# Optimization experiments

Measured on AMD Instinct MI355X. Metric: run time of the kernel, lower is better.

The kernel has to match this reference:

```python
import jax, jax.numpy as jnp
import numpy as np
import math

FACTOR = 5


def setup_inputs() -> dict:
    key = jax.random.key(0)
    k1, k2, k3, k4 = jax.random.split(key, 4)
    B, L, H, D = 8, 1024, 8, 64
    S = FACTOR * math.ceil(math.log(L))  # U_part = 35
    return {
        "queries": jax.random.normal(k1, (B, L, H, D), jnp.float32),
        "keys": jax.random.normal(k2, (B, L, H, D), jnp.float32),
        "values": jax.random.normal(k3, (B, L, H, D), jnp.float32),
        "sample_idx": jax.random.randint(k4, (L, S), 0, L, dtype=jnp.int32),
        "attn_mask": 0,  # unused by the original forward
    }


def reference(queries, keys, values, sample_idx, attn_mask):
    B, L_Q, H, D = queries.shape
    L_K = keys.shape[1]
    # [B, L, H, D] -> [B, H, L, D]
    Q = jnp.transpose(queries, (0, 2, 1, 3))
    K = jnp.transpose(keys, (0, 2, 1, 3))
    V = jnpp_transpose(values) if False else jnp.transpose(values, (0, 2, 1, 3))

    u = min(FACTOR * math.ceil(math.log(L_Q)), L_Q)  # n_top

    # --- _prob_QK: sampled scores, sparsity measure, top-u query selection ---
    K_sample = K[:, :, sample_idx, :]  # [B, H, L_Q, S, D]
    QK_sample = jnp.einsum('bhqd,bhqsd->bhqs', Q, K_sample)  # [B, H, L_Q, S]
    M = QK_sample.max(axis=-1) - QK_sample.sum(axis=-1) / L_K  # [B, H, L_Q]
    _, M_top = jax.lax.top_k(M, u)  # [B, H, u]

    Q_reduce = jnp.take_along_axis(Q, M_top[..., None], axis=2)  # [B, H, u, D]
    scale = 1.0 / math.sqrt(D)
    scores_top = jnp.einsum('bhud,bhkd->bhuk', Q_reduce, K) * scale  # [B, H, u, L_K]

    # --- initial context (mask_flag=True): running causal mean of V ---
    denom = jnp.arange(1, L_K + 1, dtype=V.dtype)[:, None]  # [L_K, 1]
    context = jnp.cumsum(V, axis=2) / denom  # [B, H, L_K, D]

    # --- softmax over keys, sparse update of selected query rows ---
    attn = jax.nn.softmax(scores_top, axis=-1)  # [B, H, u, L_K]
    update = jnp.einsum('bhuk,bhkd->bhud', attn, V)  # [B, H, u, D]

    b_idx = jnp.arange(B)[:, None, None]
    h_idx = jnp.arange(H)[None, :, None]
    context = context.at[b_idx, h_idx, M_top].set(update)

    return jnp.transpose(context, (0, 2, 1, 3))  # [B, L_Q, H, D]
```

## Files before the change

kernel.cpp:

```cpp
#include <hip/hip_runtime.h>
#include <math.h>

#define BB 8
#define LL 1024
#define HH 8
#define DD 64
#define SS 35
#define UU 35
#define BH (BB*HH)
#define CH 32
#define CROWS (LL/CH)
#define NCHK 4
#define CHK 256
#define RPAD 48

#define MBLOCKS 16384
#define C1BLOCKS (BH*CH)

typedef __attribute__((ext_vector_type(8))) short short8;
typedef __attribute__((ext_vector_type(4))) float f32x4;

__device__ __forceinline__ size_t qkv_off(int b, int l, int h, int d) {
    return (((size_t)b*LL + l)*HH + h)*DD + d;
}

__device__ __forceinline__ unsigned short f2bf(float x) {
    unsigned int u = __float_as_uint(x);
    u = (u + 0x7fffu + ((u >> 16) & 1u)) >> 16;
    return (unsigned short)u;
}

__device__ __forceinline__ short8 ld_bf8_g(const float* __restrict__ p) {
    float4 x = *reinterpret_cast<const float4*>(p);
    float4 y = *reinterpret_cast<const float4*>(p + 4);
    short8 r;
    r[0] = (short)f2bf(x.x); r[1] = (short)f2bf(x.y);
    r[2] = (short)f2bf(x.z); r[3] = (short)f2bf(x.w);
    r[4] = (short)f2bf(y.x); r[5] = (short)f2bf(y.y);
    r[6] = (short)f2bf(y.z); r[7] = (short)f2bf(y.w);
    return r;
}

__global__ __launch_bounds__(256, 4) void kernel_M_csum1(const float* __restrict__ Q,
                                                         const float* __restrict__ K,
                                                         const float* __restrict__ V,
                                                         const int*   __restrict__ sidx,
                                                         float* __restrict__ M,
                                                         float* __restrict__ csum) {
    int blk = blockIdx.x;
    if (blk < MBLOCKS) {
        int xcd  = blk & 7;
        int slot = blk >> 3;
        int bh   = ((slot >> 8) << 3) | xcd;
        int j    = slot & 255;
        int widx = threadIdx.x >> 6, lane = threadIdx.x & 63;
        int q = j * 4 + widx;
        int b = bh >> 3, h = bh & 7;
        int sub = lane & 15, grp = lane >> 4;

        const f32x4 q4 = *reinterpret_cast<const f32x4*>(Q + qkv_off(b, q, h, sub * 4));
        const int* si = sidx + q * SS;

        int idxv[9];
#pragma unroll
        for (int i = 0; i < 9; i++) {
            int s = i * 4 + grp;
            idxv[i] = si[s < SS ? s : 0];
        }
        asm volatile("" : "+v"(idxv[0]), "+v"(idxv[1]), "+v"(idxv[2]),
                          "+v"(idxv[3]), "+v"(idxv[4]), "+v"(idxv[5]),
                          "+v"(idxv[6]), "+v"(idxv[7]), "+v"(idxv[8]));

        f32x4 kv[9];
#pragma unroll
        for (int i = 0; i < 9; i++)
            kv[i] = *reinterpret_cast<const f32x4*>(K + qkv_off(b, idxv[i], h, sub * 4));
        asm volatile("" : "+v"(kv[0]), "+v"(kv[1]), "+v"(kv[2]),
                          "+v"(kv[3]), "+v"(kv[4]), "+v"(kv[5]),
                          "+v"(kv[6]), "+v"(kv[7]), "+v"(kv[8]));

        float mx = -INFINITY, sm = 0.f;
#pragma unroll
        for (int i = 0; i < 9; i++) {
            float p = q4.x * kv[i].x + q4.y * kv[i].y + q4.z * kv[i].z + q4.w * kv[i].w;
            p += __shfl_xor(p, 1);
            p += __shfl_xor(p, 2);
            p += __shfl_xor(p, 4);
            p += __shfl_xor(p, 8);
            if (i * 4 + grp < SS) { mx = fmaxf(mx, p); sm += p; }
        }
        mx = fmaxf(mx, __shfl_xor(mx, 16)); sm += __shfl_xor(sm, 16);
        mx = fmaxf(mx, __shfl_xor(mx, 32)); sm += __shfl_xor(sm, 32);
        if (lane == 0) M[bh * LL + q] = mx - sm * (1.0f / LL);
    } else {
        int blk2 = blk - MBLOCKS;
        int bh = blk2 >> 5, c = blk2 & (CH - 1);
        int b = bh >> 3, h = bh & 7;
        int d = threadIdx.x & 63, seg = threadIdx.x >> 6;
        int l0 = c * CROWS + seg * (CROWS / 4);
        const float* vp = V + qkv_off(b, l0, h, d);
        float vr[CROWS / 4];
#pragma unroll
        for (int i = 0; i < CROWS / 4; i++) vr[i] = vp[(size_t)i * (HH * DD)];
        float s = 0.f;
#pragma unroll
        for (int i = 0; i < CROWS / 4; i++) s += vr[i];
        __shared__ float red[4][64];
        red[seg][d] = s;
        __syncthreads();
        if (seg == 0)
            csum[(size_t)blk2 * 64 + d] = red[0][d] + red[1][d] + red[2][d] + red[3][d];
    }
}

__global__ __launch_bounds__(64, 4) void kernel_topk_csum2(const float* __restrict__ M,
                                                           int* __restrict__ top,
                                                           const float* __restrict__ V,
                                                           const float* __restrict__ csum,
                                                           float* __restrict__ out) {
    if (blockIdx.x < BH) {
        int bh = blockIdx.x, lane = threadIdx.x;
        float v[16];
#pragma unroll
        for (int i = 0; i < 16; i++) v[i] = M[bh * LL + i * 64 + lane];

        for (int k = 0; k < UU; k++) {
            float bv = -INFINITY; int bi = 0x7fffffff;
#pragma unroll
            for (int i = 0; i < 16; i++) {
                if (v[i] > bv) { bv = v[i]; bi = i * 64 + lane; }
            }
#pragma unroll
            for (int w = 1; w < 64; w <<= 1) {
                float ov = __shfl_xor(bv, w);
                int   oi = __shfl_xor(bi, w);
                if (ov > bv || (ov == bv && oi < bi)) { bv = ov; bi = oi; }
            }
            if (lane == 0) top[bh * UU + k] = bi;
            if ((bi & 63) == lane) {
                int slot = bi >> 6;
#pragma unroll
                for (int i = 0; i < 16; i++) if (i == slot) v[i] = -INFINITY;
            }
        }
    } else {
        int blk = blockIdx.x - BH;
        int bh = blk >> 5, c = blk & (CH - 1);
        int b = bh >> 3, h = bh & 7;
        int d = threadIdx.x;
        int l0 = c * CROWS;
        const float* vp = V + qkv_off(b, l0, h, d);

        float vr[CROWS];
#pragma unroll
        for (int i = 0; i < CROWS; i++) vr[i] = vp[(size_t)i * (HH * DD)];

        float prefix = 0.f;
#pragma unroll
        for (int cc = 0; cc < CH; cc++) {
            float vv = csum[(size_t)(bh * CH + cc) * 64 + d];
            prefix += (cc < c) ? vv : 0.f;
        }
        float* op = out + qkv_off(b, l0, h, d);
        float run = prefix;
#pragma unroll
        for (int i = 0; i < CROWS; i++) {
            run += vr[i];
            op[(size_t)i * (HH * DD)] = run / (float)(l0 + i + 1);
        }
    }
}

__global__ __launch_bounds__(256) void kernel_attn_part(const float* __restrict__ Q,
                                                        const float* __restrict__ K,
                                                        const float* __restrict__ V,
                                                        const int*   __restrict__ top,
                                                        float* __restrict__ m_ws,
                                                        float* __restrict__ se_ws,
                                                        float* __restrict__ pv_ws) {
    __shared__ unsigned short vt[64 * CHK];
    __shared__ unsigned short p_lds[RPAD * CHK];
    __shared__ float red_m[4][RPAD];
    __shared__ float red_se[4][RPAD];
    __shared__ int   qpos_s[RPAD];

    const int blk = blockIdx.x;
    const int bh  = blk >> 2;
    const int ch  = blk & 3;
    const int b   = bh >> 3, h = bh & 7;
    const int l0  = ch * CHK;
    const int tid = threadIdx.x;
    const int w    = tid >> 6;
    const int lane = tid & 63;
    const int c    = lane & 15;
    const int g    = lane >> 4;
    const float scale = 0.125f;

    if (tid < RPAD) qpos_s[tid] = top[bh * UU + (tid < UU ? tid : UU - 1)];

#pragma unroll
    for (int i = 0; i < 8; i++) {
        int task = i * 256 + tid;
        int d   = task & 63;
        int lq8 = task >> 6;
        float vv[8];
#pragma unroll
        for (int j = 0; j < 8; j++)
            vv[j] = V[qkv_off(b, l0 + lq8 * 8 + j, h, d)];
        short8 pk;
#pragma unroll
        for (int j = 0; j < 8; j++) pk[j] = (short)f2bf(vv[j]);
        *reinterpret_cast<short8*>(vt + d * CHK + (((lq8 ^ (d & 31)) << 3))) = pk;
    }
    __syncthreads();

    f32x4 acc[3][4];
#pragma unroll
    for (int mt = 0; mt < 3; mt++)
#pragma unroll
        for (int nt = 0; nt < 4; nt++) acc[mt][nt] = (f32x4){0.f, 0.f, 0.f, 0.f};

#pragma unroll
    for (int ks = 0; ks < 2; ks++) {
        int k0 = ks * 32 + g * 8;
        short8 af[3];
#pragma unroll
        for (int mt = 0; mt < 3; mt++) {
            int row = mt * 16 + c;
            af[mt] = ld_bf8_g(Q + qkv_off(b, qpos_s[row], h, k0));
        }
#pragma unroll
        for (int nt = 0; nt < 4; nt++) {
            int kl = l0 + w * 64 + nt * 16 + c;
            short8 bf = ld_bf8_g(K + qkv_off(b, kl, h, k0));
#pragma unroll
            for (int mt = 0; mt < 3; mt++)
                acc[mt][nt] = __builtin_amdgcn_mfma_f32_16x16x32_bf16(af[mt], bf, acc[mt][nt], 0, 0, 0);
        }
    }

    float tmax[3][4];
#pragma unroll
    for (int mt = 0; mt < 3; mt++)
#pragma unroll
        for (int r = 0; r < 4; r++) {
            float m = fmaxf(fmaxf(acc[mt][0][r], acc[mt][1][r]),
                            fmaxf(acc[mt][2][r], acc[mt][3][r]));
            m = fmaxf(m, __shfl_xor(m, 1));
            m = fmaxf(m, __shfl_xor(m, 2));
            m = fmaxf(m, __shfl_xor(m, 4));
            m = fmaxf(m, __shfl_xor(m, 8));
            tmax[mt][r] = m;
        }
    if (c == 0) {
#pragma unroll
        for (int mt = 0; mt < 3; mt++)
#pragma unroll
            for (int r = 0; r < 4; r++)
                red_m[w][mt * 16 + g * 4 + r] = tmax[mt][r];
    }
    __syncthreads();

    float tse[3][4];
#pragma unroll
    for (int mt = 0; mt < 3; mt++)
#pragma unroll
        for (int r = 0; r < 4; r++) {
            int row = mt * 16 + g * 4 + r;
            float m = fmaxf(fmaxf(red_m[0][row], red_m[1][row]),
                            fmaxf(red_m[2][row], red_m[3][row]));
            float s = 0.f;
#pragma unroll
            for (int nt = 0; nt < 4; nt++) {
                float p = __expf(scale * (acc[mt][nt][r] - m));
                acc[mt][nt][r] = p;
                s += p;
                p_lds[row * CHK + w * 64 + nt * 16 + c] = f2bf(p);
            }
            s += __shfl_xor(s, 1);
            s += __shfl_xor(s, 2);
            s += __shfl_xor(s, 4);
            s += __shfl_xor(s, 8);
            tse[mt][r] = s;
        }
    if (c == 0) {
#pragma unroll
        for (int mt = 0; mt < 3; mt++)
#pragma unroll
            for (int r = 0; r < 4; r++)
                red_se[w][mt * 16 + g * 4 + r] = tse[mt][r];
    }
    __syncthreads();

    if (tid < RPAD) {
        float mm = fmaxf(fmaxf(red_m[0][tid], red_m[1][tid]),
                         fmaxf(red_m[2][tid], red_m[3][tid]));
        float ss = red_se[0][tid] + red_se[1][tid] + red_se[2][tid] + red_se[3][tid];
        m_ws[blk * RPAD + tid]  = mm;
        se_ws[blk * RPAD + tid] = ss;
    }

    f32x4 acc2[3];
#pragma unroll
    for (int mt = 0; mt < 3; mt++) acc2[mt] = (f32x4){0.f, 0.f, 0.f, 0.f};

#pragma unroll
    for (int ks = 0; ks < 8; ks++) {
        int slot = ks * 4 + g;
        int d    = w * 16 + c;
        short8 bf = *reinterpret_cast<const short8*>(
            vt + d * CHK + ((slot ^ (d & 31)) << 3));
#pragma unroll
        for (int mt = 0; mt < 3; mt++) {
            short8 af = *reinterpret_cast<const short8*>(
                p_lds + (mt * 16 + c) * CHK + ks * 32 + g * 8);
            acc2[mt] = __builtin_amdgcn_mfma_f32_16x16x32_bf16(af, bf, acc2[mt], 0, 0, 0);
        }
    }

#pragma unroll
    for (int mt = 0; mt < 3; mt++)
#pragma unroll
        for (int r = 0; r < 4; r++) {
            int row = mt * 16 + g * 4 + r;
            pv_ws[((size_t)blk * RPAD + row) * 64 + w * 16 + c] = acc2[mt][r];
        }
}

__global__ __launch_bounds__(256) void kernel_attn_comb(const int* __restrict__ top,
                                                        const float* __restrict__ m_ws,
                                                        const float* __restrict__ se_ws,
                                                        const float* __restrict__ pv_ws,
                                                        float* __restrict__ out) {
    int bh = blockIdx.x;
    int b = bh >> 3, h = bh & 7;
    const float scale = 0.125f;
    for (int idx = threadIdx.x; idx < UU * 64; idx += 256) {
        int r = idx >> 6, d = idx & 63;
        float mc[NCHK];
        float mm = -INFINITY;
#pragma unroll
        for (int ch = 0; ch < NCHK; ch++) {
            mc[ch] = m_ws[(bh * NCHK + ch) * RPAD + r];
            mm = fmaxf(mm, mc[ch]);
        }
        float num = 0.f, den = 0.f;
#pragma unroll
        for (int ch = 0; ch < NCHK; ch++) {
            float f = __expf(scale * (mc[ch] - mm));
            num += f * pv_ws[((size_t)(bh * NCHK + ch) * RPAD + r) * 64 + d];
            den += f * se_ws[(bh * NCHK + ch) * RPAD + r];
        }
        out[qkv_off(b, top[bh * UU + r], h, d)] = num / den;
    }
}

extern "C" void kernel_launch(void* const* d_in, const int* in_sizes, int n_in,
                              void* d_out, int out_size, void* d_ws, size_t ws_size,
                              hipStream_t stream) {
    const float* Q    = (const float*)d_in[0];
    const float* K    = (const float*)d_in[1];
    const float* V    = (const float*)d_in[2];
    const int*   sidx = (const int*)d_in[3];
    float* out = (float*)d_out;

    char* ws = (char*)d_ws;
    float* M     = (float*)(ws);
    int*   top   = (int*)  (ws + 262144);
    float* csum  = (float*)(ws + 271360);
    float* m_ws  = (float*)(ws + 795648);
    float* se_ws = (float*)(ws + 844800);
    float* pv_ws = (float*)(ws + 893952);

    kernel_M_csum1  <<<MBLOCKS + C1BLOCKS, 256, 0, stream>>>(Q, K, V, sidx, M, csum);
    kernel_topk_csum2<<<BH + C1BLOCKS, 64, 0, stream>>>(M, top, V, csum, out);
    kernel_attn_part<<<BH * NCHK, 256, 0, stream>>>(Q, K, V, top, m_ws, se_ws, pv_ws);
    kernel_attn_comb<<<BH, 256, 0, stream>>>(top, m_ws, se_ws, pv_ws, out);
}
```

Baseline: 81.66 us.

## Process two queries per wave in M kernel with DPP row reductions

The sampled-score kernel now handles two query rows per wavefront, which halves the M block count and doubles the independent K gathers in flight per wave. Lane-group sample assignment becomes contiguous (each 16-lane group takes 9 consecutive samples), and the cross-lane sums switch from shfl_xor to DPP row operations. Index math is simplified to shifts, and launch bounds drop to 3 waves per SIMD to leave room for the extra registers, which may lower occupancy.

```diff
diff --git a/kernel.cpp b/kernel.cpp
--- a/kernel.cpp
+++ b/kernel.cpp
@@ -14,7 +14,7 @@
 #define CHK 256
 #define RPAD 48
 
-#define MBLOCKS 16384
+#define MBLOCKS2 8192
 #define C1BLOCKS (BH*CH)
 
 typedef __attribute__((ext_vector_type(8))) short short8;
@@ -41,59 +41,92 @@
     return r;
 }
 
-__global__ __launch_bounds__(256, 4) void kernel_M_csum1(const float* __restrict__ Q,
+__device__ __forceinline__ float row16_sum(float p) {
+    int t;
+    t = __builtin_amdgcn_update_dpp(0, __float_as_int(p), 0xB1, 0xF, 0xF, true);
+    p += __int_as_float(t);
+    t = __builtin_amdgcn_update_dpp(0, __float_as_int(p), 0x4E, 0xF, 0xF, true);
+    p += __int_as_float(t);
+    t = __builtin_amdgcn_update_dpp(0, __float_as_int(p), 0x141, 0xF, 0xF, true);
+    p += __int_as_float(t);
+    t = __builtin_amdgcn_update_dpp(0, __float_as_int(p), 0x140, 0xF, 0xF, true);
+    p += __int_as_float(t);
+    return p;
+}
+
+__global__ __launch_bounds__(256, 3) void kernel_M_csum1(const float* __restrict__ Q,
                                                          const float* __restrict__ K,
                                                          const float* __restrict__ V,
                                                          const int*   __restrict__ sidx,
                                                          float* __restrict__ M,
                                                          float* __restrict__ csum) {
     int blk = blockIdx.x;
-    if (blk < MBLOCKS) {
+    if (blk < MBLOCKS2) {
         int xcd  = blk & 7;
         int slot = blk >> 3;
-        int bh   = ((slot >> 8) << 3) | xcd;
-        int j    = slot & 255;
+        int bh   = ((slot >> 7) << 3) | xcd;
+        int j    = slot & 127;
         int widx = threadIdx.x >> 6, lane = threadIdx.x & 63;
-        int q = j * 4 + widx;
+        int q0   = j * 8 + widx * 2;
         int b = bh >> 3, h = bh & 7;
-        int sub = lane & 15, grp = lane >> 4;
-
-        const f32x4 q4 = *reinterpret_cast<const f32x4*>(Q + qkv_off(b, q, h, sub * 4));
-        const int* si = sidx + q * SS;
-
-        int idxv[9];
+        int sub = lane & 15, g = lane >> 4;
+
+        int base = (((b << 13) + h) << 6) + (sub << 2);
+        const f32x4 qa = *reinterpret_cast<const f32x4*>(Q + base + (q0 << 9));
+        const f32x4 qb = *reinterpret_cast<const f32x4*>(Q + base + ((q0 + 1) << 9));
+
+        const int* sia = sidx + q0 * SS + g * 9;
+        const int* sib = sia + SS;
+
+        int ia[9], ib[9];
 #pragma unroll
         for (int i = 0; i < 9; i++) {
-            int s = i * 4 + grp;
-            idxv[i] = si[s < SS ? s : 0];
-        }
-        asm volatile("" : "+v"(idxv[0]), "+v"(idxv[1]), "+v"(idxv[2]),
-                          "+v"(idxv[3]), "+v"(idxv[4]), "+v"(idxv[5]),
-                          "+v"(idxv[6]), "+v"(idxv[7]), "+v"(idxv[8]));
-
-        f32x4 kv[9];
+            int ii = (i == 8 && g == 3) ? 7 : i;
+            ia[i] = sia[ii];
+            ib[i] = sib[ii];
+        }
+
+        f32x4 ka[9], kb[9];
 #pragma unroll
         for (int i = 0; i < 9; i++)
-            kv[i] = *reinterpret_cast<const f32x4*>(K + qkv_off(b, idxv[i], h, sub * 4));
-        asm volatile("" : "+v"(kv[0]), "+v"(kv[1]), "+v"(kv[2]),
-                          "+v"(kv[3]), "+v"(kv[4]), "+v"(kv[5]),
-                          "+v"(kv[6]), "+v"(kv[7]), "+v"(kv[8]));
-
-        float mx = -INFINITY, sm = 0.f;
+            ka[i] = *reinterpret_cast<const f32x4*>(K + base + ((unsigned)ia[i] << 9));
+#pragma unroll
+        for (int i = 0; i < 9; i++)
+            kb[i] = *reinterpret_cast<const f32x4*>(K + base + ((unsigned)ib[i] << 9));
+
+        float mxa = 0.f, sma = 0.f, mxb = 0.f, smb = 0.f;
 #pragma unroll
         for (int i = 0; i < 9; i++) {
-            float p = q4.x * kv[i].x + q4.y * kv[i].y + q4.z * kv[i].z + q4.w * kv[i].w;
-            p += __shfl_xor(p, 1);
-            p += __shfl_xor(p, 2);
-            p += __shfl_xor(p, 4);
-            p += __shfl_xor(p, 8);
-            if (i * 4 + grp < SS) { mx = fmaxf(mx, p); sm += p; }
-        }
-        mx = fmaxf(mx, __shfl_xor(mx, 16)); sm += __shfl_xor(sm, 16);
-        mx = fmaxf(mx, __shfl_xor(mx, 32)); sm += __shfl_xor(sm, 32);
-        if (lane == 0) M[bh * LL + q] = mx - sm * (1.0f / LL);
+            float p = qa.x * ka[i].x + qa.y * ka[i].y + qa.z * ka[i].z + qa.w * ka[i].w;
+            p = row16_sum(p);
+            if (i == 0)      { mxa = p; sma = p; }
+            else if (i < 8)  { mxa = fmaxf(mxa, p); sma += p; }
+            else             { bool v = (g < 3);
+                               mxa = fmaxf(mxa, v ? p : -INFINITY);
+                               sma += v ? p : 0.f; }
+        }
+#pragma unroll
+        for (int i = 0; i < 9; i++) {
+            float p = qb.x * kb[i].x + qb.y * kb[i].y + qb.z * kb[i].z + qb.w * kb[i].w;
+            p = row16_sum(p);
+            if (i == 0)      { mxb = p; smb = p; }
+            else if (i < 8)  { mxb = fmaxf(mxb, p); smb += p; }
+            else             { bool v = (g < 3);
+                               mxb = fmaxf(mxb, v ? p : -INFINITY);
+                               smb += v ? p : 0.f; }
+        }
+
+        mxa = fmaxf(mxa, __shfl_xor(mxa, 16)); sma += __shfl_xor(sma, 16);
+        mxa = fmaxf(mxa, __shfl_xor(mxa, 32)); sma += __shfl_xor(sma, 32);
+        mxb = fmaxf(mxb, __shfl_xor(mxb, 16)); smb += __shfl_xor(smb, 16);
+        mxb = fmaxf(mxb, __shfl_xor(mxb, 32)); smb += __shfl_xor(smb, 32);
+
+        if (lane == 0) {
+            M[bh * LL + q0]     = mxa - sma * (1.0f / LL);
+            M[bh * LL + q0 + 1] = mxb - smb * (1.0f / LL);
+        }
     } else {
-        int blk2 = blk - MBLOCKS;
+        int blk2 = blk - MBLOCKS2;
         int bh = blk2 >> 5, c = blk2 & (CH - 1);
         int b = bh >> 3, h = bh & 7;
         int d = threadIdx.x & 63, seg = threadIdx.x >> 6;
@@ -372,8 +405,8 @@
     float* se_ws = (float*)(ws + 844800);
     float* pv_ws = (float*)(ws + 893952);
 
-    kernel_M_csum1  <<<MBLOCKS + C1BLOCKS, 256, 0, stream>>>(Q, K, V, sidx, M, csum);
+    kernel_M_csum1   <<<MBLOCKS2 + C1BLOCKS, 256, 0, stream>>>(Q, K, V, sidx, M, csum);
     kernel_topk_csum2<<<BH + C1BLOCKS, 64, 0, stream>>>(M, top, V, csum, out);
-    kernel_attn_part<<<BH * NCHK, 256, 0, stream>>>(Q, K, V, top, m_ws, se_ws, pv_ws);
-    kernel_attn_comb<<<BH, 256, 0, stream>>>(top, m_ws, se_ws, pv_ws, out);
-}
+    kernel_attn_part <<<BH * NCHK, 256, 0, stream>>>(Q, K, V, top, m_ws, se_ws, pv_ws);
+    kernel_attn_comb <<<BH, 256, 0, stream>>>(top, m_ws, se_ws, pv_ws, out);
+}
```

Result: no change. 80.44 us (-1.5%).
